# Performance work log

Hardware: AMD Instinct MI355X
Metric: run time of the kernel (lower is better)

## Reference

```python
import jax, jax.numpy as jnp
import numpy as np

B, N, ATTR, H, OUT, STEPS = 8, 4096, 16, 64, 1, 8


def setup_inputs() -> dict:
    key = jax.random.key(0)
    ks = jax.random.split(key, 12)
    attr_matrix = jax.random.normal(ks[0], (B, N, ATTR), jnp.float32)
    adj_matrix = (jax.random.uniform(ks[1], (B, N, N)) < 0.01).astype(jnp.float32)
    s = float(1.0 / np.sqrt(H))
    u = lambda k, shape: jax.random.uniform(k, shape, jnp.float32, -s, s)
    Wi = jax.random.normal(ks[2], (H, ATTR), jnp.float32) * float(np.sqrt(2.0 / ATTR))  # kaiming
    bi = jnp.zeros((H,), jnp.float32)
    Wz = u(ks[3], (H, 3 * H)); bz = u(ks[4], (H,))
    Wr = u(ks[5], (H, 3 * H)); br = u(ks[6], (H,))
    Wh = u(ks[7], (H, 3 * H)); bh = u(ks[8], (H,))
    Wo = jax.random.normal(ks[9], (OUT, H), jnp.float32) * float(np.sqrt(2.0 / (H + OUT)))  # xavier
    bo = jnp.zeros((OUT,), jnp.float32)
    return dict(attr_matrix=attr_matrix, adj_matrix=adj_matrix, Wi=Wi, bi=bi,
                Wz=Wz, bz=bz, Wr=Wr, br=br, Wh=Wh, bh=bh, Wo=Wo, bo=bo)


def reference(attr_matrix, adj_matrix, Wi, bi, Wz, bz, Wr, br, Wh, bh, Wo, bo):
    # initial node states: (B, N, H)
    h = jax.nn.relu(attr_matrix @ Wi.T + bi)
    A_in = adj_matrix
    A_out = jnp.swapaxes(adj_matrix, -1, -2)
    for _ in range(STEPS):
        a_in = jnp.einsum('bij,bjh->bih', A_in, h)
        a_out = jnp.einsum('bij,bjh->bih', A_out, h)
        inp = jnp.concatenate([a_in, a_out], axis=-1)           # (B, N, 2H)
        xs = jnp.concatenate([inp, h], axis=-1)                  # (B, N, 3H)
        z = jax.nn.sigmoid(xs @ Wz.T + bz)
        r = jax.nn.sigmoid(xs @ Wr.T + br)
        hn = jnp.tanh(jnp.concatenate([inp, r * h], axis=-1) @ Wh.T + bh)
        h = (1.0 - z) * h + z * hn
    return h @ Wo.T + bo  # (B, N, OUT)
```

## Files before the change

kernel.cpp:

```cpp
#include <hip/hip_runtime.h>
#include <hip/hip_fp16.h>
#include <stdint.h>

#define BB 8
#define NN 4096
#define ATTRD 16
#define HD 64
#define STEPS 8
#define NODES (BB*NN)
#define ECAP 96
#define KPAD 196

typedef _Float16 half8 __attribute__((ext_vector_type(8)));
typedef float floatx4 __attribute__((ext_vector_type(4)));
typedef unsigned long long ull;

__global__ void init_h_kernel(const float* __restrict__ attr, const float* __restrict__ Wi,
                              const float* __restrict__ bi, float* __restrict__ h,
                              __half* __restrict__ h16) {
    int idx = blockIdx.x * blockDim.x + threadIdx.x;
    if (idx >= NODES * HD) return;
    int node = idx >> 6, l = idx & 63;
    const float* a = attr + node * ATTRD;
    const float* w = Wi + l * ATTRD;
    float acc = bi[l];
#pragma unroll
    for (int k = 0; k < ATTRD; k++) acc += a[k] * w[k];
    float r = acc > 0.f ? acc : 0.f;
    h[idx] = r;
    h16[idx] = __float2half(r);
}

__global__ void wprep_kernel(const float* __restrict__ Wz, const float* __restrict__ Wr,
                             const float* __restrict__ Wh,
                             _Float16* __restrict__ wf_hi, _Float16* __restrict__ wf_lo) {
    int t = blockIdx.x * blockDim.x + threadIdx.x;
    if (t >= 3 * 4 * 6 * 64 * 8) return;
    int mat = t / 12288, rem = t % 12288;
    int tile = rem / 3072, rem2 = rem % 3072;
    int kc = rem2 / 512, rem3 = rem2 % 512;
    int lane = rem3 / 8, j = rem3 % 8;
    int k = kc * 32 + (lane >> 4) * 8 + j;
    int och = tile * 16 + (lane & 15);
    const float* W = (mat == 0) ? Wz : (mat == 1) ? Wr : Wh;
    float v = W[och * 192 + k];
    _Float16 hi = (_Float16)v;
    wf_hi[t] = hi;
    wf_lo[t] = (_Float16)(v - (float)hi);
}

__global__ void count_fill_kernel(const float4* __restrict__ A4,
                                  int* __restrict__ cnt_in, int* __restrict__ cnt_out,
                                  int* __restrict__ edge_in, int* __restrict__ edge_out) {
    int tid0 = blockIdx.x * blockDim.x + threadIdx.x;
    const int stride = gridDim.x * blockDim.x;
    int l = threadIdx.x & 63;
    ull mask_lt = (l == 63) ? ~0ull >> 1 : ((1ull << (l + 1)) - 1) >> 1;
#pragma unroll 1
    for (int o = 0; o < 4; o++) {
        int idx[4]; float4 v[4];
#pragma unroll
        for (int c = 0; c < 4; c++) idx[c] = tid0 + (o * 4 + c) * stride;
#pragma unroll
        for (int c = 0; c < 4; c++) v[c] = A4[idx[c]];
        ull b[4][4]; int tot[4]; int row[4];
#pragma unroll
        for (int c = 0; c < 4; c++) {
            b[c][0] = __ballot(v[c].x != 0.f);
            b[c][1] = __ballot(v[c].y != 0.f);
            b[c][2] = __ballot(v[c].z != 0.f);
            b[c][3] = __ballot(v[c].w != 0.f);
            tot[c] = __popcll(b[c][0]) + __popcll(b[c][1]) +
                     __popcll(b[c][2]) + __popcll(b[c][3]);
            row[c] = idx[c] >> 10;
        }
        int myTot = (l == 1) ? tot[1] : (l == 2) ? tot[2] : (l == 3) ? tot[3] : tot[0];
        int myRow = (l == 1) ? row[1] : (l == 2) ? row[2] : (l == 3) ? row[3] : row[0];
        int res = 0;
        if (l < 4 && myTot) res = atomicAdd(&cnt_in[myRow], myTot);
        int base[4];
#pragma unroll
        for (int c = 0; c < 4; c++) base[c] = __shfl(res, c);
#pragma unroll
        for (int c = 0; c < 4; c++) {
            if (!tot[c]) continue;
            int e = idx[c] * 4;
            int colbase = (e >> 24) << 12;
            int pre = __popcll(b[c][0] & mask_lt) + __popcll(b[c][1] & mask_lt) +
                      __popcll(b[c][2] & mask_lt) + __popcll(b[c][3] & mask_lt);
            float vv[4] = {v[c].x, v[c].y, v[c].z, v[c].w};
            int inner = 0;
#pragma unroll
            for (int q = 0; q < 4; q++) {
                if (vv[q] != 0.f) {
                    int s1 = base[c] + pre + inner;
                    if (s1 < ECAP) edge_in[row[c] * ECAP + s1] = colbase | ((e + q) & 4095);
                    inner++;
                }
            }
        }
#pragma unroll
        for (int c = 0; c < 4; c++) {
            if (!tot[c]) continue;
            int e = idx[c] * 4;
            int colbase = (e >> 24) << 12;
            float vv[4] = {v[c].x, v[c].y, v[c].z, v[c].w};
#pragma unroll
            for (int q = 0; q < 4; q++) {
                if (vv[q] != 0.f) {
                    int col = colbase | ((e + q) & 4095);
                    int s2 = atomicAdd(&cnt_out[col], 1);
                    if (s2 < ECAP) edge_out[col * ECAP + s2] = row[c];
                }
            }
        }
    }
}

__global__ __launch_bounds__(256) void aggregate_kernel(
        const __half2* __restrict__ h2, const float* __restrict__ h,
        const int* __restrict__ cnt_in, const int* __restrict__ edge_in,
        const int* __restrict__ cnt_out, const int* __restrict__ edge_out,
        float* __restrict__ xs) {
    int bid = blockIdx.x;
    int batch = bid & 7;
    int group = bid >> 3;
    int wave = threadIdx.x >> 6;
    int pair = group * 4 + wave;
    int node = (batch << 12) + (pair >> 1);
    int dir = pair & 1;
    int l = threadIdx.x & 63;
    int half = l >> 5, sl = l & 31;
    int n = dir ? cnt_out[node] : cnt_in[node];
    if (n > ECAP) n = ECAP;
    const int* eidx = (dir ? edge_out : edge_in) + node * ECAP;
    float a0 = 0.f, a1 = 0.f;
    int s = 0;
    for (; s + 16 <= n; s += 16) {
        int i0 = eidx[s +  0 + half];
        int i1 = eidx[s +  2 + half];
        int i2 = eidx[s +  4 + half];
        int i3 = eidx[s +  6 + half];
        int i4 = eidx[s +  8 + half];
        int i5 = eidx[s + 10 + half];
        int i6 = eidx[s + 12 + half];
        int i7 = eidx[s + 14 + half];
        float2 f0 = __half22float2(h2[(i0 << 5) | sl]);
        float2 f1 = __half22float2(h2[(i1 << 5) | sl]);
        float2 f2 = __half22float2(h2[(i2 << 5) | sl]);
        float2 f3 = __half22float2(h2[(i3 << 5) | sl]);
        float2 f4 = __half22float2(h2[(i4 << 5) | sl]);
        float2 f5 = __half22float2(h2[(i5 << 5) | sl]);
        float2 f6 = __half22float2(h2[(i6 << 5) | sl]);
        float2 f7 = __half22float2(h2[(i7 << 5) | sl]);
        a0 += f0.x; a1 += f0.y;  a0 += f1.x; a1 += f1.y;
        a0 += f2.x; a1 += f2.y;  a0 += f3.x; a1 += f3.y;
        a0 += f4.x; a1 += f4.y;  a0 += f5.x; a1 += f5.y;
        a0 += f6.x; a1 += f6.y;  a0 += f7.x; a1 += f7.y;
    }
    for (; s + 8 <= n; s += 8) {
        int i0 = eidx[s + 0 + half];
        int i1 = eidx[s + 2 + half];
        int i2 = eidx[s + 4 + half];
        int i3 = eidx[s + 6 + half];
        float2 f0 = __half22float2(h2[(i0 << 5) | sl]);
        float2 f1 = __half22float2(h2[(i1 << 5) | sl]);
        float2 f2 = __half22float2(h2[(i2 << 5) | sl]);
        float2 f3 = __half22float2(h2[(i3 << 5) | sl]);
        a0 += f0.x; a1 += f0.y;  a0 += f1.x; a1 += f1.y;
        a0 += f2.x; a1 += f2.y;  a0 += f3.x; a1 += f3.y;
    }
    for (; s + 2 <= n; s += 2) {
        float2 f0 = __half22float2(h2[(eidx[s + half] << 5) | sl]);
        a0 += f0.x; a1 += f0.y;
    }
    if (s < n && half == 0) {
        float2 f0 = __half22float2(h2[(eidx[s] << 5) | sl]);
        a0 += f0.x; a1 += f0.y;
    }
    a0 += __shfl_xor(a0, 32);
    a1 += __shfl_xor(a1, 32);
    if (half == 0) {
        float2 st = {a0, a1};
        *(float2*)(xs + node * 192 + dir * 64 + sl * 2) = st;
    }
    if (dir == 0) xs[node * 192 + 128 + l] = h[(node << 6) | l];
}

__global__ __launch_bounds__(256) void gate_kernel(
        const float* __restrict__ xs_g,
        const _Float16* __restrict__ wf_hi, const _Float16* __restrict__ wf_lo,
        const float* __restrict__ bz, const float* __restrict__ br,
        const float* __restrict__ bh,
        float* __restrict__ h, __half* __restrict__ h16) {
    __shared__ float xs_t[16][KPAD];
    int bid = blockIdx.x;
    int base = ((bid & 7) << 12) | ((bid >> 3) << 4);
    int tid = threadIdx.x;
    {
        const float4* src = (const float4*)(xs_g + base * 192);
#pragma unroll
        for (int i = 0; i < 3; i++) {
            int idx = tid + i * 256;
            float4 v = src[idx];
            int nl = idx / 48, kb = (idx % 48) * 4;
            *(float4*)&xs_t[nl][kb] = v;
        }
    }
    __syncthreads();
    int wave = tid >> 6, lane = tid & 63;
    int m = lane & 15, q = lane >> 4;
    int ch = wave * 16 + m;
    const half8* WH = (const half8*)wf_hi;
    const half8* WL = (const half8*)wf_lo;

    floatx4 accz = {0.f, 0.f, 0.f, 0.f};
    floatx4 accr = {0.f, 0.f, 0.f, 0.f};
#pragma unroll
    for (int kc = 0; kc < 6; kc++) {
        const float* xr = &xs_t[m][kc * 32 + q * 8];
        float4 xa = *(const float4*)xr;
        float4 xb = *(const float4*)(xr + 4);
        float xv[8] = {xa.x, xa.y, xa.z, xa.w, xb.x, xb.y, xb.z, xb.w};
        half8 ahi, alo;
#pragma unroll
        for (int j = 0; j < 8; j++) {
            _Float16 hj = (_Float16)xv[j];
            ahi[j] = hj;
            alo[j] = (_Float16)(xv[j] - (float)hj);
        }
        half8 bzh = WH[((0 * 4 + wave) * 6 + kc) * 64 + lane];
        half8 bzl = WL[((0 * 4 + wave) * 6 + kc) * 64 + lane];
        half8 brh = WH[((1 * 4 + wave) * 6 + kc) * 64 + lane];
        half8 brl = WL[((1 * 4 + wave) * 6 + kc) * 64 + lane];
        accz = __builtin_amdgcn_mfma_f32_16x16x32_f16(ahi, bzh, accz, 0, 0, 0);
        accz = __builtin_amdgcn_mfma_f32_16x16x32_f16(alo, bzh, accz, 0, 0, 0);
        accz = __builtin_amdgcn_mfma_f32_16x16x32_f16(ahi, bzl, accz, 0, 0, 0);
        accr = __builtin_amdgcn_mfma_f32_16x16x32_f16(ahi, brh, accr, 0, 0, 0);
        accr = __builtin_amdgcn_mfma_f32_16x16x32_f16(alo, brh, accr, 0, 0, 0);
        accr = __builtin_amdgcn_mfma_f32_16x16x32_f16(ahi, brl, accr, 0, 0, 0);
    }
    float bzv = bz[ch], brv = br[ch], bhv = bh[ch];
    float zreg[4], hvreg[4], rh[4];
#pragma unroll
    for (int rg = 0; rg < 4; rg++) {
        int nl = q * 4 + rg;
        float z = 1.f / (1.f + __expf(-(accz[rg] + bzv)));
        float r = 1.f / (1.f + __expf(-(accr[rg] + brv)));
        float hv = xs_t[nl][128 + ch];
        zreg[rg] = z; hvreg[rg] = hv; rh[rg] = r * hv;
    }
    __syncthreads();
#pragma unroll
    for (int rg = 0; rg < 4; rg++) xs_t[q * 4 + rg][128 + ch] = rh[rg];
    __syncthreads();

    floatx4 acch = {0.f, 0.f, 0.f, 0.f};
#pragma unroll
    for (int kc = 0; kc < 6; kc++) {
        const float* xr = &xs_t[m][kc * 32 + q * 8];
        float4 xa = *(const float4*)xr;
        float4 xb = *(const float4*)(xr + 4);
        float xv[8] = {xa.x, xa.y, xa.z, xa.w, xb.x, xb.y, xb.z, xb.w};
        half8 ahi, alo;
#pragma unroll
        for (int j = 0; j < 8; j++) {
            _Float16 hj = (_Float16)xv[j];
            ahi[j] = hj;
            alo[j] = (_Float16)(xv[j] - (float)hj);
        }
        half8 bhh = WH[((2 * 4 + wave) * 6 + kc) * 64 + lane];
        half8 bhl = WL[((2 * 4 + wave) * 6 + kc) * 64 + lane];
        acch = __builtin_amdgcn_mfma_f32_16x16x32_f16(ahi, bhh, acch, 0, 0, 0);
        acch = __builtin_amdgcn_mfma_f32_16x16x32_f16(alo, bhh, acch, 0, 0, 0);
        acch = __builtin_amdgcn_mfma_f32_16x16x32_f16(ahi, bhl, acch, 0, 0, 0);
    }
    __syncthreads();
#pragma unroll
    for (int rg = 0; rg < 4; rg++) {
        int nl = q * 4 + rg;
        float pre = acch[rg] + bhv;
        float th = 2.f / (1.f + __expf(-2.f * pre)) - 1.f;
        float hv = hvreg[rg];
        xs_t[nl][ch] = hv + zreg[rg] * (th - hv);
    }
    __syncthreads();
    {
        int f = tid * 4;
        int nl = f >> 6, c = f & 63;
        float4 v = *(const float4*)&xs_t[nl][c];
        int gi = ((base + nl) << 6) | c;
        *(float4*)&h[gi] = v;
        __half2 p0 = {__float2half(v.x), __float2half(v.y)};
        __half2 p1 = {__float2half(v.z), __float2half(v.w)};
        *(__half2*)&h16[gi] = p0;
        *(__half2*)&h16[gi + 2] = p1;
    }
}

__global__ void out_kernel(const float* __restrict__ h, const float* __restrict__ Wo,
                           const float* __restrict__ bo, float* __restrict__ out) {
    int wid = (blockIdx.x * blockDim.x + threadIdx.x) >> 6;
    int l = threadIdx.x & 63;
    if (wid >= NODES) return;
    float p = h[(wid << 6) | l] * Wo[l];
#pragma unroll
    for (int off = 32; off > 0; off >>= 1) p += __shfl_down(p, off);
    if (l == 0) out[wid] = p + bo[0];
}

extern "C" void kernel_launch(void* const* d_in, const int* in_sizes, int n_in,
                              void* d_out, int out_size, void* d_ws, size_t ws_size,
                              hipStream_t stream) {
    const float* attr = (const float*)d_in[0];
    const float* adj  = (const float*)d_in[1];
    const float* Wi   = (const float*)d_in[2];
    const float* bi   = (const float*)d_in[3];
    const float* Wz   = (const float*)d_in[4];
    const float* bz   = (const float*)d_in[5];
    const float* Wr   = (const float*)d_in[6];
    const float* br   = (const float*)d_in[7];
    const float* Wh   = (const float*)d_in[8];
    const float* bh   = (const float*)d_in[9];
    const float* Wo   = (const float*)d_in[10];
    const float* bo   = (const float*)d_in[11];
    float* out = (float*)d_out;

    char* ws = (char*)d_ws;
    size_t off = 0;
    auto carve = [&](size_t bytes) { void* p = ws + off; off = (off + bytes + 255) & ~(size_t)255; return p; };
    float* h      = (float*)carve((size_t)NODES * HD * 4);
    __half* h16   = (__half*)carve((size_t)NODES * HD * 2);
    float* xs     = (float*)carve((size_t)NODES * 192 * 4);
    _Float16* wf_hi = (_Float16*)carve(3 * 4 * 6 * 64 * 8 * 2);
    _Float16* wf_lo = (_Float16*)carve(3 * 4 * 6 * 64 * 8 * 2);
    int* cnt_in   = (int*)carve((size_t)2 * NODES * 4);
    int* cnt_out  = cnt_in + NODES;
    int* edge_in  = (int*)carve((size_t)NODES * ECAP * 4);
    int* edge_out = (int*)carve((size_t)NODES * ECAP * 4);

    hipMemsetAsync(cnt_in, 0, (size_t)2 * NODES * 4, stream);

    init_h_kernel<<<NODES * HD / 256, 256, 0, stream>>>(attr, Wi, bi, h, h16);
    wprep_kernel<<<(3 * 4 * 6 * 64 * 8 + 255) / 256, 256, 0, stream>>>(Wz, Wr, Wh, wf_hi, wf_lo);
    count_fill_kernel<<<8192, 256, 0, stream>>>((const float4*)adj, cnt_in, cnt_out,
                                                edge_in, edge_out);

    for (int step = 0; step < STEPS; ++step) {
        aggregate_kernel<<<NODES * 2 * 64 / 256, 256, 0, stream>>>(
            (const __half2*)h16, h, cnt_in, edge_in, cnt_out, edge_out, xs);
        gate_kernel<<<NODES / 16, 256, 0, stream>>>(xs, wf_hi, wf_lo, bz, br, bh, h, h16);
    }
    out_kernel<<<NODES * HD / 256, 256, 0, stream>>>(h, Wo, bo, out);
}
```

Baseline: 1.259 ms.

## Build adjacency lists row-per-wave and derive out-edges via separate transpose kernel

Replaces the grid-strided count/fill kernel with one wave per adjacency row that scans the whole row, computes slots by running ballot prefix counts, and writes cnt_in directly without atomics. Out-edge lists are then built in a second kernel that reads the compact in-edge lists, so the dense matrix is scanned once and per-nonzero atomics on cnt_out come from a much smaller input. This removes the per-chunk atomics on cnt_in and interleaved scatter work from the dense pass. It adds a kernel launch and holds 16 float4 loads per lane in registers, which may lower occupancy.

```diff
diff --git a/kernel.cpp b/kernel.cpp
--- a/kernel.cpp
+++ b/kernel.cpp
@@ -49,71 +49,54 @@
     wf_lo[t] = (_Float16)(v - (float)hi);
 }
 
-__global__ void count_fill_kernel(const float4* __restrict__ A4,
-                                  int* __restrict__ cnt_in, int* __restrict__ cnt_out,
-                                  int* __restrict__ edge_in, int* __restrict__ edge_out) {
-    int tid0 = blockIdx.x * blockDim.x + threadIdx.x;
-    const int stride = gridDim.x * blockDim.x;
-    int l = threadIdx.x & 63;
+__global__ __launch_bounds__(256) void count_rows_kernel(const float4* __restrict__ A4,
+                                                         int* __restrict__ cnt_in,
+                                                         int* __restrict__ edge_in) {
+    int wave = threadIdx.x >> 6, l = threadIdx.x & 63;
+    int row = blockIdx.x * 4 + wave;
+    const float4* rp = A4 + (size_t)row * 1024;
     ull mask_lt = (l == 63) ? ~0ull >> 1 : ((1ull << (l + 1)) - 1) >> 1;
-#pragma unroll 1
-    for (int o = 0; o < 4; o++) {
-        int idx[4]; float4 v[4];
-#pragma unroll
-        for (int c = 0; c < 4; c++) idx[c] = tid0 + (o * 4 + c) * stride;
-#pragma unroll
-        for (int c = 0; c < 4; c++) v[c] = A4[idx[c]];
-        ull b[4][4]; int tot[4]; int row[4];
-#pragma unroll
-        for (int c = 0; c < 4; c++) {
-            b[c][0] = __ballot(v[c].x != 0.f);
-            b[c][1] = __ballot(v[c].y != 0.f);
-            b[c][2] = __ballot(v[c].z != 0.f);
-            b[c][3] = __ballot(v[c].w != 0.f);
-            tot[c] = __popcll(b[c][0]) + __popcll(b[c][1]) +
-                     __popcll(b[c][2]) + __popcll(b[c][3]);
-            row[c] = idx[c] >> 10;
-        }
-        int myTot = (l == 1) ? tot[1] : (l == 2) ? tot[2] : (l == 3) ? tot[3] : tot[0];
-        int myRow = (l == 1) ? row[1] : (l == 2) ? row[2] : (l == 3) ? row[3] : row[0];
-        int res = 0;
-        if (l < 4 && myTot) res = atomicAdd(&cnt_in[myRow], myTot);
-        int base[4];
-#pragma unroll
-        for (int c = 0; c < 4; c++) base[c] = __shfl(res, c);
-#pragma unroll
-        for (int c = 0; c < 4; c++) {
-            if (!tot[c]) continue;
-            int e = idx[c] * 4;
-            int colbase = (e >> 24) << 12;
-            int pre = __popcll(b[c][0] & mask_lt) + __popcll(b[c][1] & mask_lt) +
-                      __popcll(b[c][2] & mask_lt) + __popcll(b[c][3] & mask_lt);
-            float vv[4] = {v[c].x, v[c].y, v[c].z, v[c].w};
-            int inner = 0;
-#pragma unroll
-            for (int q = 0; q < 4; q++) {
-                if (vv[q] != 0.f) {
-                    int s1 = base[c] + pre + inner;
-                    if (s1 < ECAP) edge_in[row[c] * ECAP + s1] = colbase | ((e + q) & 4095);
-                    inner++;
-                }
+    float4 v[16];
+#pragma unroll
+    for (int t = 0; t < 16; t++) v[t] = rp[t * 64 + l];
+    int colbase = (row >> 12) << 12;
+    int run = 0;
+    int* erow = edge_in + row * ECAP;
+#pragma unroll
+    for (int t = 0; t < 16; t++) {
+        ull b0 = __ballot(v[t].x != 0.f);
+        ull b1 = __ballot(v[t].y != 0.f);
+        ull b2 = __ballot(v[t].z != 0.f);
+        ull b3 = __ballot(v[t].w != 0.f);
+        int pre = __popcll(b0 & mask_lt) + __popcll(b1 & mask_lt) +
+                  __popcll(b2 & mask_lt) + __popcll(b3 & mask_lt);
+        float vv[4] = {v[t].x, v[t].y, v[t].z, v[t].w};
+        int jbase = (t * 64 + l) * 4;
+        int inner = 0;
+#pragma unroll
+        for (int q = 0; q < 4; q++) {
+            if (vv[q] != 0.f) {
+                int slot = run + pre + inner;
+                if (slot < ECAP) erow[slot] = colbase | (jbase + q);
+                inner++;
             }
         }
-#pragma unroll
-        for (int c = 0; c < 4; c++) {
-            if (!tot[c]) continue;
-            int e = idx[c] * 4;
-            int colbase = (e >> 24) << 12;
-            float vv[4] = {v[c].x, v[c].y, v[c].z, v[c].w};
-#pragma unroll
-            for (int q = 0; q < 4; q++) {
-                if (vv[q] != 0.f) {
-                    int col = colbase | ((e + q) & 4095);
-                    int s2 = atomicAdd(&cnt_out[col], 1);
-                    if (s2 < ECAP) edge_out[col * ECAP + s2] = row[c];
-                }
-            }
-        }
+        run += __popcll(b0) + __popcll(b1) + __popcll(b2) + __popcll(b3);
+    }
+    if (l == 0) cnt_in[row] = run;
+}
+
+__global__ __launch_bounds__(256) void transpose_kernel(const int* __restrict__ cnt_in,
+                                                        const int* __restrict__ edge_in,
+                                                        int* __restrict__ cnt_out,
+                                                        int* __restrict__ edge_out) {
+    int wave = threadIdx.x >> 6, l = threadIdx.x & 63;
+    int row = blockIdx.x * 4 + wave;
+    int n = cnt_in[row]; if (n > ECAP) n = ECAP;
+    for (int s = l; s < n; s += 64) {
+        int j = edge_in[row * ECAP + s];
+        int s2 = atomicAdd(&cnt_out[j], 1);
+        if (s2 < ECAP) edge_out[j * ECAP + s2] = row;
     }
 }
 
@@ -334,17 +317,17 @@
     float* xs     = (float*)carve((size_t)NODES * 192 * 4);
     _Float16* wf_hi = (_Float16*)carve(3 * 4 * 6 * 64 * 8 * 2);
     _Float16* wf_lo = (_Float16*)carve(3 * 4 * 6 * 64 * 8 * 2);
-    int* cnt_in   = (int*)carve((size_t)2 * NODES * 4);
-    int* cnt_out  = cnt_in + NODES;
+    int* cnt_in   = (int*)carve((size_t)NODES * 4);
+    int* cnt_out  = (int*)carve((size_t)NODES * 4);
     int* edge_in  = (int*)carve((size_t)NODES * ECAP * 4);
     int* edge_out = (int*)carve((size_t)NODES * ECAP * 4);
 
-    hipMemsetAsync(cnt_in, 0, (size_t)2 * NODES * 4, stream);
+    hipMemsetAsync(cnt_out, 0, (size_t)NODES * 4, stream);
 
     init_h_kernel<<<NODES * HD / 256, 256, 0, stream>>>(attr, Wi, bi, h, h16);
     wprep_kernel<<<(3 * 4 * 6 * 64 * 8 + 255) / 256, 256, 0, stream>>>(Wz, Wr, Wh, wf_hi, wf_lo);
-    count_fill_kernel<<<8192, 256, 0, stream>>>((const float4*)adj, cnt_in, cnt_out,
-                                                edge_in, edge_out);
+    count_rows_kernel<<<NODES / 4, 256, 0, stream>>>((const float4*)adj, cnt_in, edge_in);
+    transpose_kernel<<<NODES / 4, 256, 0, stream>>>(cnt_in, edge_in, cnt_out, edge_out);
 
     for (int step = 0; step < STEPS; ++step) {
         aggregate_kernel<<<NODES * 2 * 64 / 256, 256, 0, stream>>>(
```

Measured after the change: 1.255 ms. About the same (-0.3%).
